# Kernel optimization log

Hardware: AMD Instinct MI355X
Metric: run time of the kernel (lower is better)

Reference implementation:

```python
import jax, jax.numpy as jnp
import numpy as np


def setup_inputs() -> dict:
    key = jax.random.key(0)
    kE, kD, kW, kU, kV = jax.random.split(key, 5)
    B, T, H, U = 32, 2048, 1024, 1024
    scale = 0.02
    return {
        "enc_out": jax.random.normal(kE, (B, T, H), dtype=jnp.float32),
        "dec_hidden": jax.random.normal(kD, (B, H), dtype=jnp.float32),
        "Wa": jax.random.normal(kW, (H, U), dtype=jnp.float32) * scale,
        "Ua": jax.random.normal(kU, (H, U), dtype=jnp.float32) * scale,
        "Va": jax.random.normal(kV, (U,), dtype=jnp.float32) * scale,
    }


def reference(enc_out, dec_hidden, Wa, Ua, Va):
    # Bahdanau additive attention.
    # enc_out: [B, T, H]; dec_hidden: [B, H]; Wa: [H, U]; Ua: [H, U]; Va: [U]
    dec_proj = jnp.einsum("bh,hu->bu", dec_hidden, Wa)          # [B, U]
    enc_proj = jnp.einsum("bth,hu->btu", enc_out, Ua)            # [B, T, U]
    s = jnp.tanh(enc_proj + dec_proj[:, None, :])                # [B, T, U]
    score = jnp.einsum("btu,u->bt", s, Va)                       # [B, T]
    alpha = jax.nn.softmax(score, axis=-1)                       # [B, T]
    context = jnp.einsum("bt,bth->bh", alpha, enc_out)           # [B, H]
    return context
```

## Files before the change

### kernel.cpp

```cpp
#include <hip/hip_runtime.h>
#include <stdint.h>


#define B_ 32
#define T_ 2048
#define H_ 1024
#define U_ 1024
#define M_ (B_ * T_)

typedef __bf16 bf16x8 __attribute__((ext_vector_type(8)));
typedef float f32x4 __attribute__((ext_vector_type(4)));

__device__ __forceinline__ unsigned f2b(float f) {
  unsigned u = __float_as_uint(f);
  return (u + 0x7FFFu + ((u >> 16) & 1u)) >> 16;
}
__device__ __forceinline__ float b2f(unsigned short u) {
  return __uint_as_float(((unsigned)u) << 16);
}
__device__ __forceinline__ float fast_tanh(float x) {
  float xc = fminf(fmaxf(x, -12.f), 12.f);
  float t = exp2f(xc * 2.885390081777927f);
  return (t - 1.f) * __builtin_amdgcn_rcpf(t + 1.f);
}

#define AS1 __attribute__((address_space(1)))
#define AS3 __attribute__((address_space(3)))
__device__ __forceinline__ void gld_lds16(const void* g, void* l) {
  __builtin_amdgcn_global_load_lds((AS1 const void*)g, (AS3 void*)l, 16, 0, 0);
}

__global__ __launch_bounds__(256) void conv_enc_k(const float4* __restrict__ in,
                                                  uint4* __restrict__ out) {
  size_t i = (size_t)blockIdx.x * 256 + threadIdx.x;
  float4 a = in[i * 2], b = in[i * 2 + 1];
  uint4 o;
  o.x = f2b(a.x) | (f2b(a.y) << 16);
  o.y = f2b(a.z) | (f2b(a.w) << 16);
  o.z = f2b(b.x) | (f2b(b.y) << 16);
  o.w = f2b(b.z) | (f2b(b.w) << 16);
  out[i] = o;
}

__global__ __launch_bounds__(256) void conv_ua_k(const float* __restrict__ in,
                                                 unsigned short* __restrict__ out) {
  int id = blockIdx.x * 256 + threadIdx.x;
  int h = id >> 10, u = id & 1023;
  out[(((size_t)(h >> 3) * U_ + u) << 3) + (h & 7)] = (unsigned short)f2b(in[id]);
}

__global__ __launch_bounds__(64) void decproj_k(const float* __restrict__ dh,
                                                const float* __restrict__ Wa,
                                                float* __restrict__ dp) {
  int u = blockIdx.x * 64 + threadIdx.x;
  int b = blockIdx.y;
  const float* d = dh + b * H_;
  const float* w = Wa + u;
  float acc = 0.f;
#pragma unroll 8
  for (int h = 0; h < H_; ++h) acc = fmaf(d[h], w[(size_t)h * U_], acc);
  dp[b * U_ + u] = acc;
}

__global__ __launch_bounds__(256, 2) void score_gemm_k(
    const unsigned short* __restrict__ encb,
    const unsigned short* __restrict__ Ub,
    const float* __restrict__ dp,
    const float* __restrict__ Va,
    float* __restrict__ score)
{
  __shared__ alignas(16) unsigned short As[8][128][8];
  __shared__ alignas(16) unsigned short Bs[8][128][8];

  const int bx = blockIdx.x;
  const int mtile = bx & 511, ntile = bx >> 9;
  const int m0 = mtile << 7, n0 = ntile << 7;
  const int tid = threadIdx.x;
  const int wv = tid >> 6, ln = tid & 63;
  const int wm = wv & 1, wn = wv >> 1;
  const int quad = ln >> 4, l16 = ln & 15;

  f32x4 acc[4][4];
  const f32x4 zero = {0.f, 0.f, 0.f, 0.f};
#pragma unroll
  for (int i = 0; i < 4; ++i)
#pragma unroll
    for (int j = 0; j < 4; ++j) acc[i][j] = zero;

  for (int k0 = 0; k0 < H_; k0 += 64) {
    __syncthreads();
#pragma unroll
    for (int c = 0; c < 4; ++c) {
      int chunk = (wv << 2) + c;
      int k8 = chunk >> 1, half = chunk & 1;
      const unsigned short* ga =
          encb + (size_t)(m0 + (half << 6) + ln) * H_ + k0 + (k8 << 3);
      gld_lds16(ga, &As[k8][half << 6][0]);
      const unsigned short* gb =
          Ub + (((size_t)((k0 >> 3) + k8) * U_) + n0 + (half << 6) + ln) * 8;
      gld_lds16(gb, &Bs[k8][half << 6][0]);
    }
    __syncthreads();

#pragma unroll
    for (int kk = 0; kk < 2; ++kk) {
      int k8b = (kk << 2) + quad;
      bf16x8 af[4], bf[4];
#pragma unroll
      for (int mt = 0; mt < 4; ++mt)
        af[mt] = *(const bf16x8*)&As[k8b][(wm << 6) + (mt << 4) + l16][0];
#pragma unroll
      for (int nt = 0; nt < 4; ++nt)
        bf[nt] = *(const bf16x8*)&Bs[k8b][(wn << 6) + (nt << 4) + l16][0];
#pragma unroll
      for (int mt = 0; mt < 4; ++mt)
#pragma unroll
        for (int nt = 0; nt < 4; ++nt)
          acc[mt][nt] = __builtin_amdgcn_mfma_f32_16x16x32_bf16(
              af[mt], bf[nt], acc[mt][nt], 0, 0, 0);
    }
  }

  const int bq = m0 >> 11;
  float va[4], dpv[4];
#pragma unroll
  for (int nt = 0; nt < 4; ++nt) {
    int col = n0 + (wn << 6) + (nt << 4) + l16;
    va[nt] = Va[col];
    dpv[nt] = dp[bq * U_ + col];
  }
#pragma unroll
  for (int mt = 0; mt < 4; ++mt) {
#pragma unroll
    for (int r = 0; r < 4; ++r) {
      float v = 0.f;
#pragma unroll
      for (int nt = 0; nt < 4; ++nt)
        v += fast_tanh(acc[mt][nt][r] + dpv[nt]) * va[nt];
      v += __shfl_xor(v, 1);
      v += __shfl_xor(v, 2);
      v += __shfl_xor(v, 4);
      v += __shfl_xor(v, 8);
      if (l16 == 0)
        atomicAdd(&score[m0 + (wm << 6) + (mt << 4) + (quad << 2) + r], v);
    }
  }
}

__global__ __launch_bounds__(256) void softmax_k(float* __restrict__ score) {
  const int b = blockIdx.x, tid = threadIdx.x;
  float4* s4 = (float4*)(score + b * T_);
  __shared__ float red[4];
  float4 v0 = s4[tid * 2], v1 = s4[tid * 2 + 1];
  float m = fmaxf(fmaxf(fmaxf(v0.x, v0.y), fmaxf(v0.z, v0.w)),
                  fmaxf(fmaxf(v1.x, v1.y), fmaxf(v1.z, v1.w)));
#pragma unroll
  for (int off = 32; off >= 1; off >>= 1) m = fmaxf(m, __shfl_xor(m, off));
  if ((tid & 63) == 0) red[tid >> 6] = m;
  __syncthreads();
  m = fmaxf(fmaxf(red[0], red[1]), fmaxf(red[2], red[3]));
  __syncthreads();
  const float l2e = 1.4426950408889634f;
  float e[8];
  e[0] = exp2f((v0.x - m) * l2e); e[1] = exp2f((v0.y - m) * l2e);
  e[2] = exp2f((v0.z - m) * l2e); e[3] = exp2f((v0.w - m) * l2e);
  e[4] = exp2f((v1.x - m) * l2e); e[5] = exp2f((v1.y - m) * l2e);
  e[6] = exp2f((v1.z - m) * l2e); e[7] = exp2f((v1.w - m) * l2e);
  float sum = e[0] + e[1] + e[2] + e[3] + e[4] + e[5] + e[6] + e[7];
#pragma unroll
  for (int off = 32; off >= 1; off >>= 1) sum += __shfl_xor(sum, off);
  if ((tid & 63) == 0) red[tid >> 6] = sum;
  __syncthreads();
  float inv = 1.f / (red[0] + red[1] + red[2] + red[3]);
  v0.x = e[0] * inv; v0.y = e[1] * inv; v0.z = e[2] * inv; v0.w = e[3] * inv;
  v1.x = e[4] * inv; v1.y = e[5] * inv; v1.z = e[6] * inv; v1.w = e[7] * inv;
  s4[tid * 2] = v0;
  s4[tid * 2 + 1] = v1;
}

__global__ __launch_bounds__(256) void context_k(const unsigned short* __restrict__ encb,
                                                 const float* __restrict__ alpha,
                                                 float* __restrict__ out) {
  const int b = blockIdx.y, tch = blockIdx.x;
  const int h4 = threadIdx.x << 2;
  const unsigned short* base = encb + (size_t)b * T_ * H_ + h4;
  const float* al = alpha + b * T_ + tch * 256;
  float a0 = 0.f, a1 = 0.f, a2 = 0.f, a3 = 0.f;
  for (int t = 0; t < 256; ++t) {
    float a = al[t];
    ushort4 e = *(const ushort4*)(base + (size_t)(tch * 256 + t) * H_);
    a0 = fmaf(a, b2f(e.x), a0);
    a1 = fmaf(a, b2f(e.y), a1);
    a2 = fmaf(a, b2f(e.z), a2);
    a3 = fmaf(a, b2f(e.w), a3);
  }
  float* o = out + b * H_ + h4;
  atomicAdd(o + 0, a0); atomicAdd(o + 1, a1);
  atomicAdd(o + 2, a2); atomicAdd(o + 3, a3);
}

extern "C" void kernel_launch(void* const* d_in, const int* in_sizes, int n_in,
                              void* d_out, int out_size, void* d_ws, size_t ws_size,
                              hipStream_t stream) {
  const float* enc = (const float*)d_in[0];
  const float* dh  = (const float*)d_in[1];
  const float* Wa  = (const float*)d_in[2];
  const float* Ua  = (const float*)d_in[3];
  const float* Va  = (const float*)d_in[4];
  float* out = (float*)d_out;

  char* ws = (char*)d_ws;
  unsigned short* encb = (unsigned short*)ws;
  unsigned short* Ub   = (unsigned short*)(ws + 134217728);
  float* dp    = (float*)(ws + 134217728 + 2097152);
  float* score = (float*)(ws + 134217728 + 2097152 + 131072);

  hipMemsetAsync(score, 0, M_ * sizeof(float), stream);
  hipMemsetAsync(d_out, 0, B_ * H_ * sizeof(float), stream);

  conv_enc_k<<<32768, 256, 0, stream>>>((const float4*)enc, (uint4*)encb);
  conv_ua_k<<<4096, 256, 0, stream>>>(Ua, Ub);
  decproj_k<<<dim3(16, 32), 64, 0, stream>>>(dh, Wa, dp);
  score_gemm_k<<<4096, 256, 0, stream>>>(encb, Ub, dp, Va, score);
  softmax_k<<<32, 256, 0, stream>>>(score);
  context_k<<<dim3(8, 32), 256, 0, stream>>>(encb, score, out);
}
```

Measured before the change: 693.7 us.

## Pre-tile encoder bf16 layout for contiguous GEMM loads and rework reductions

The encoder conversion kernel now writes bf16 data in a tiled layout of 128-row by k8-chunk blocks, so the score GEMM's global-to-LDS loads for A read contiguous 2KB runs instead of strided rows. The context kernel is rewritten to read this tiled layout with 16-byte loads. The score epilogue replaces per-row shuffle reductions and many atomics with an LDS reduction that issues one atomic per row. The decoder projection is split over H with atomics for more parallelism. The conversion kernel's writes become scattered, and the context kernel now reads tiled rows, which may affect how well its accesses coalesce.

```diff
diff --git a/kernel.cpp b/kernel.cpp
--- a/kernel.cpp
+++ b/kernel.cpp
@@ -31,15 +31,25 @@
 }
 
 __global__ __launch_bounds__(256) void conv_enc_k(const float4* __restrict__ in,
-                                                  uint4* __restrict__ out) {
-  size_t i = (size_t)blockIdx.x * 256 + threadIdx.x;
-  float4 a = in[i * 2], b = in[i * 2 + 1];
-  uint4 o;
-  o.x = f2b(a.x) | (f2b(a.y) << 16);
-  o.y = f2b(a.z) | (f2b(a.w) << 16);
-  o.z = f2b(b.x) | (f2b(b.y) << 16);
-  o.w = f2b(b.z) | (f2b(b.w) << 16);
-  out[i] = o;
+                                                  uint4* __restrict__ outA) {
+  const int ml = threadIdx.x & 127, kh = threadIdx.x >> 7;
+  const int bk = blockIdx.x;
+  const int mt = blockIdx.y;
+  const int kc = bk * 2 + kh;
+  const float4* src = in + ((size_t)(mt * 128 + ml) * 256) + kc * 4;
+  float4 a = src[0], b = src[1], c = src[2], d = src[3];
+  uint4 o0, o1;
+  o0.x = f2b(a.x) | (f2b(a.y) << 16);
+  o0.y = f2b(a.z) | (f2b(a.w) << 16);
+  o0.z = f2b(b.x) | (f2b(b.y) << 16);
+  o0.w = f2b(b.z) | (f2b(b.w) << 16);
+  o1.x = f2b(c.x) | (f2b(c.y) << 16);
+  o1.y = f2b(c.z) | (f2b(c.w) << 16);
+  o1.z = f2b(d.x) | (f2b(d.y) << 16);
+  o1.w = f2b(d.z) | (f2b(d.w) << 16);
+  const int k8 = kc * 2;
+  outA[((size_t)mt * 128 + k8) * 128 + ml] = o0;
+  outA[((size_t)mt * 128 + k8 + 1) * 128 + ml] = o1;
 }
 
 __global__ __launch_bounds__(256) void conv_ua_k(const float* __restrict__ in,
@@ -49,28 +59,38 @@
   out[(((size_t)(h >> 3) * U_ + u) << 3) + (h & 7)] = (unsigned short)f2b(in[id]);
 }
 
-__global__ __launch_bounds__(64) void decproj_k(const float* __restrict__ dh,
-                                                const float* __restrict__ Wa,
-                                                float* __restrict__ dp) {
-  int u = blockIdx.x * 64 + threadIdx.x;
-  int b = blockIdx.y;
-  const float* d = dh + b * H_;
-  const float* w = Wa + u;
-  float acc = 0.f;
-#pragma unroll 8
-  for (int h = 0; h < H_; ++h) acc = fmaf(d[h], w[(size_t)h * U_], acc);
-  dp[b * U_ + u] = acc;
+__global__ __launch_bounds__(256) void decproj_k(const float* __restrict__ dh,
+                                                 const float* __restrict__ Wa,
+                                                 float* __restrict__ dp) {
+  const int u = blockIdx.x * 256 + threadIdx.x;
+  const int b = blockIdx.y, hz = blockIdx.z;
+  const float* d = dh + b * H_ + hz * 256;
+  const float* w = Wa + (size_t)(hz * 256) * U_ + u;
+  float a0 = 0.f, a1 = 0.f, a2 = 0.f, a3 = 0.f;
+#pragma unroll 4
+  for (int h = 0; h < 256; h += 4) {
+    a0 = fmaf(d[h + 0], w[(size_t)(h + 0) * U_], a0);
+    a1 = fmaf(d[h + 1], w[(size_t)(h + 1) * U_], a1);
+    a2 = fmaf(d[h + 2], w[(size_t)(h + 2) * U_], a2);
+    a3 = fmaf(d[h + 3], w[(size_t)(h + 3) * U_], a3);
+  }
+  atomicAdd(&dp[b * U_ + u], (a0 + a1) + (a2 + a3));
 }
 
 __global__ __launch_bounds__(256, 2) void score_gemm_k(
-    const unsigned short* __restrict__ encb,
+    const unsigned short* __restrict__ encA,
     const unsigned short* __restrict__ Ub,
     const float* __restrict__ dp,
     const float* __restrict__ Va,
     float* __restrict__ score)
 {
-  __shared__ alignas(16) unsigned short As[8][128][8];
-  __shared__ alignas(16) unsigned short Bs[8][128][8];
+  __shared__ union {
+    struct {
+      alignas(16) unsigned short As[8][128][8];
+      alignas(16) unsigned short Bs[8][128][8];
+    } t;
+    float sred[128 * 33];
+  } sm;
 
   const int bx = blockIdx.x;
   const int mtile = bx & 511, ntile = bx >> 9;
@@ -87,6 +107,8 @@
 #pragma unroll
     for (int j = 0; j < 4; ++j) acc[i][j] = zero;
 
+  const unsigned short* encT = encA + (size_t)mtile * (128 * 128 * 8);
+
   for (int k0 = 0; k0 < H_; k0 += 64) {
     __syncthreads();
 #pragma unroll
@@ -94,11 +116,11 @@
       int chunk = (wv << 2) + c;
       int k8 = chunk >> 1, half = chunk & 1;
       const unsigned short* ga =
-          encb + (size_t)(m0 + (half << 6) + ln) * H_ + k0 + (k8 << 3);
-      gld_lds16(ga, &As[k8][half << 6][0]);
+          encT + (((size_t)((k0 >> 3) + k8) * 128) + (half << 6) + ln) * 8;
+      gld_lds16(ga, &sm.t.As[k8][half << 6][0]);
       const unsigned short* gb =
           Ub + (((size_t)((k0 >> 3) + k8) * U_) + n0 + (half << 6) + ln) * 8;
-      gld_lds16(gb, &Bs[k8][half << 6][0]);
+      gld_lds16(gb, &sm.t.Bs[k8][half << 6][0]);
     }
     __syncthreads();
 
@@ -108,10 +130,10 @@
       bf16x8 af[4], bf[4];
 #pragma unroll
       for (int mt = 0; mt < 4; ++mt)
-        af[mt] = *(const bf16x8*)&As[k8b][(wm << 6) + (mt << 4) + l16][0];
+        af[mt] = *(const bf16x8*)&sm.t.As[k8b][(wm << 6) + (mt << 4) + l16][0];
 #pragma unroll
       for (int nt = 0; nt < 4; ++nt)
-        bf[nt] = *(const bf16x8*)&Bs[k8b][(wn << 6) + (nt << 4) + l16][0];
+        bf[nt] = *(const bf16x8*)&sm.t.Bs[k8b][(wn << 6) + (nt << 4) + l16][0];
 #pragma unroll
       for (int mt = 0; mt < 4; ++mt)
 #pragma unroll
@@ -129,6 +151,7 @@
     va[nt] = Va[col];
     dpv[nt] = dp[bq * U_ + col];
   }
+  __syncthreads();
 #pragma unroll
   for (int mt = 0; mt < 4; ++mt) {
 #pragma unroll
@@ -137,13 +160,17 @@
 #pragma unroll
       for (int nt = 0; nt < 4; ++nt)
         v += fast_tanh(acc[mt][nt][r] + dpv[nt]) * va[nt];
-      v += __shfl_xor(v, 1);
-      v += __shfl_xor(v, 2);
-      v += __shfl_xor(v, 4);
-      v += __shfl_xor(v, 8);
-      if (l16 == 0)
-        atomicAdd(&score[m0 + (wm << 6) + (mt << 4) + (quad << 2) + r], v);
+      int row = (wm << 6) + (mt << 4) + (quad << 2) + r;
+      sm.sred[row * 33 + (wn << 4) + l16] = v;
     }
+  }
+  __syncthreads();
+  if (tid < 128) {
+    const float* p = &sm.sred[tid * 33];
+    float s = 0.f;
+#pragma unroll
+    for (int j = 0; j < 32; ++j) s += p[j];
+    atomicAdd(&score[m0 + tid], s);
   }
 }
 
@@ -166,7 +193,7 @@
   e[2] = exp2f((v0.z - m) * l2e); e[3] = exp2f((v0.w - m) * l2e);
   e[4] = exp2f((v1.x - m) * l2e); e[5] = exp2f((v1.y - m) * l2e);
   e[6] = exp2f((v1.z - m) * l2e); e[7] = exp2f((v1.w - m) * l2e);
-  float sum = e[0] + e[1] + e[2] + e[3] + e[4] + e[5] + e[6] + e[7];
+  float sum = (e[0] + e[1]) + (e[2] + e[3]) + (e[4] + e[5]) + (e[6] + e[7]);
 #pragma unroll
   for (int off = 32; off >= 1; off >>= 1) sum += __shfl_xor(sum, off);
   if ((tid & 63) == 0) red[tid >> 6] = sum;
@@ -178,25 +205,39 @@
   s4[tid * 2 + 1] = v1;
 }
 
-__global__ __launch_bounds__(256) void context_k(const unsigned short* __restrict__ encb,
+__global__ __launch_bounds__(256) void context_k(const uint4* __restrict__ encA,
                                                  const float* __restrict__ alpha,
                                                  float* __restrict__ out) {
-  const int b = blockIdx.y, tch = blockIdx.x;
-  const int h4 = threadIdx.x << 2;
-  const unsigned short* base = encb + (size_t)b * T_ * H_ + h4;
-  const float* al = alpha + b * T_ + tch * 256;
-  float a0 = 0.f, a1 = 0.f, a2 = 0.f, a3 = 0.f;
-  for (int t = 0; t < 256; ++t) {
-    float a = al[t];
-    ushort4 e = *(const ushort4*)(base + (size_t)(tch * 256 + t) * H_);
-    a0 = fmaf(a, b2f(e.x), a0);
-    a1 = fmaf(a, b2f(e.y), a1);
-    a2 = fmaf(a, b2f(e.z), a2);
-    a3 = fmaf(a, b2f(e.w), a3);
-  }
-  float* o = out + b * H_ + h4;
-  atomicAdd(o + 0, a0); atomicAdd(o + 1, a1);
-  atomicAdd(o + 2, a2); atomicAdd(o + 3, a3);
+  const int tx = threadIdx.x & 127, th = threadIdx.x >> 7;
+  const int b = blockIdx.y, bt = blockIdx.x;
+  const int mt = b * 16 + bt;
+  const uint4* base = encA + ((size_t)mt * 128 + tx) * 128 + th * 64;
+  const float* al = alpha + b * T_ + bt * 128 + th * 64;
+  float a[8];
+#pragma unroll
+  for (int j = 0; j < 8; ++j) a[j] = 0.f;
+#pragma unroll 4
+  for (int i = 0; i < 64; ++i) {
+    float w = al[i];
+    uint4 e = base[i];
+    a[0] = fmaf(w, b2f((unsigned short)e.x), a[0]);
+    a[1] = fmaf(w, b2f((unsigned short)(e.x >> 16)), a[1]);
+    a[2] = fmaf(w, b2f((unsigned short)e.y), a[2]);
+    a[3] = fmaf(w, b2f((unsigned short)(e.y >> 16)), a[3]);
+    a[4] = fmaf(w, b2f((unsigned short)e.z), a[4]);
+    a[5] = fmaf(w, b2f((unsigned short)(e.z >> 16)), a[5]);
+    a[6] = fmaf(w, b2f((unsigned short)e.w), a[6]);
+    a[7] = fmaf(w, b2f((unsigned short)(e.w >> 16)), a[7]);
+  }
+  __shared__ float cred[2][128][8];
+#pragma unroll
+  for (int j = 0; j < 8; ++j) cred[th][tx][j] = a[j];
+  __syncthreads();
+  if (th == 0) {
+#pragma unroll
+    for (int j = 0; j < 8; ++j)
+      atomicAdd(&out[b * H_ + tx * 8 + j], cred[0][tx][j] + cred[1][tx][j]);
+  }
 }
 
 extern "C" void kernel_launch(void* const* d_in, const int* in_sizes, int n_in,
@@ -207,21 +248,21 @@
   const float* Wa  = (const float*)d_in[2];
   const float* Ua  = (const float*)d_in[3];
   const float* Va  = (const float*)d_in[4];
-  float* out = (float*)d_out;
 
   char* ws = (char*)d_ws;
-  unsigned short* encb = (unsigned short*)ws;
+  unsigned short* encA = (unsigned short*)ws;
   unsigned short* Ub   = (unsigned short*)(ws + 134217728);
   float* dp    = (float*)(ws + 134217728 + 2097152);
   float* score = (float*)(ws + 134217728 + 2097152 + 131072);
 
+  hipMemsetAsync(dp, 0, B_ * U_ * sizeof(float), stream);
   hipMemsetAsync(score, 0, M_ * sizeof(float), stream);
   hipMemsetAsync(d_out, 0, B_ * H_ * sizeof(float), stream);
 
-  conv_enc_k<<<32768, 256, 0, stream>>>((const float4*)enc, (uint4*)encb);
+  conv_enc_k<<<dim3(32, 512), 256, 0, stream>>>((const float4*)enc, (uint4*)encA);
   conv_ua_k<<<4096, 256, 0, stream>>>(Ua, Ub);
-  decproj_k<<<dim3(16, 32), 64, 0, stream>>>(dh, Wa, dp);
-  score_gemm_k<<<4096, 256, 0, stream>>>(encb, Ub, dp, Va, score);
+  decproj_k<<<dim3(4, 32, 4), 256, 0, stream>>>(dh, Wa, dp);
+  score_gemm_k<<<4096, 256, 0, stream>>>(encA, Ub, dp, Va, score);
   softmax_k<<<32, 256, 0, stream>>>(score);
-  context_k<<<dim3(8, 32), 256, 0, stream>>>(encb, score, out);
-}
+  context_k<<<dim3(16, 32), 256, 0, stream>>>((const uint4*)encA, score, (float*)d_out);
+}
```

Result: faster. 626.9 us (-9.6%).
